# Kernel optimization log

Hardware: AMD Instinct MI355X
Metric: run time of the kernel (lower is better)

Reference implementation:

```python
import jax, jax.numpy as jnp
import numpy as np

D_MODEL = 1024
LAYER_IDX = 5
D_FF = 4096
SPARSITY = 0.9
TOKENS = 8192
IN_UP = D_MODEL * (LAYER_IDX + 1)  # 6144


def _sparse_weight(rng, out_f, in_f, sparsity):
    """Row-wise k-sparse weight matrix mimicking SparseLinear's padded-CSR:
    each output row keeps k = round(in_f*(1-sparsity)) live columns,
    values ~ U(-b, b) with b = 1/sqrt(effective_fan_in)."""
    k = max(1, round(in_f * (1.0 - sparsity)))
    bound = 1.0 / np.sqrt(max(1.0, in_f * (1.0 - sparsity)))
    scores = rng.random((out_f, in_f))
    # top-k per row -> boolean mask
    thresh = np.partition(scores, in_f - k, axis=1)[:, in_f - k][:, None]
    mask = scores >= thresh
    W = (rng.uniform(-bound, bound, (out_f, in_f)).astype(np.float32)) * mask
    return jnp.asarray(W), jnp.asarray(mask)


def setup_inputs() -> dict:
    key = jax.random.key(0)
    x = jax.random.normal(key, (TOKENS, IN_UP), dtype=jnp.float32)
    rng = np.random.default_rng(0)
    W_up, mask_up = _sparse_weight(rng, D_FF, IN_UP, SPARSITY)
    W_down, mask_down = _sparse_weight(rng, D_MODEL, D_FF, SPARSITY)
    return {"ffn_input_cat": x, "W_up": W_up, "W_down": W_down,
            "mask_up": mask_up, "mask_down": mask_down}


def reference(ffn_input_cat, W_up, W_down, mask_up, mask_down):
    # fc_down(gelu(fc_up(x))); SparseLinear == masked dense linear, no bias.
    # torch F.gelu default is the exact (erf) gelu.
    h = jax.nn.gelu(ffn_input_cat @ (W_up * mask_up).T, approximate=False)  # [T, d_ff]
    return h @ (W_down * mask_down).T  # [T, d_model]
```

## Files before the change

kernel.cpp:

```cpp
#include <hip/hip_runtime.h>
#include <cstdint>
#include <cstddef>

typedef unsigned short u16;
typedef __attribute__((ext_vector_type(8))) short  bf16x8;
typedef __attribute__((ext_vector_type(4))) float  f32x4;

__device__ __forceinline__ u16 f2bf(float f) {
    unsigned u = __float_as_uint(f);
    unsigned r = (u + 0x7FFFu + ((u >> 16) & 1u)) >> 16;
    return (u16)r;
}

__device__ __forceinline__ void async_lds16(const u16* g, u16* l) {
    __builtin_amdgcn_global_load_lds(
        (const __attribute__((address_space(1))) unsigned int*)g,
        (__attribute__((address_space(3))) unsigned int*)l,
        16, 0, 0);
}

__global__ __launch_bounds__(256) void cvt3_kernel(const float* __restrict__ s0, u16* __restrict__ d0, int n0,
                                                   const float* __restrict__ s1, u16* __restrict__ d1, int n1,
                                                   const float* __restrict__ s2, u16* __restrict__ d2, int n2) {
    int i = blockIdx.x * 256 + threadIdx.x;
    const float* s; u16* d;
    if (i < n0)            { s = s0; d = d0; }
    else if (i < n0 + n1)  { s = s1; d = d1; i -= n0; }
    else                   { s = s2; d = d2; i -= n0 + n1; if (i >= n2) return; }
    const float4* sp = (const float4*)s;
    float4 a = sp[2 * i];
    float4 b = sp[2 * i + 1];
    union { bf16x8 v; u16 e[8]; } o;
    o.e[0] = f2bf(a.x); o.e[1] = f2bf(a.y); o.e[2] = f2bf(a.z); o.e[3] = f2bf(a.w);
    o.e[4] = f2bf(b.x); o.e[5] = f2bf(b.y); o.e[6] = f2bf(b.z); o.e[7] = f2bf(b.w);
    ((bf16x8*)d)[i] = o.v;
}

#define BM 128
#define BN 128
#define BK 64

template<bool GELU, typename OutT>
__global__ __launch_bounds__(256) void gemm_bt(const u16* __restrict__ A,
                                               const u16* __restrict__ B,
                                               OutT* __restrict__ C,
                                               int M, int N, int K,
                                               int lda, int ldb, int ldc) {
    __shared__ __align__(16) u16 As[BM * BK];
    __shared__ __align__(16) u16 Bs[BN * BK];

    const int tid  = threadIdx.x;
    const int wave = tid >> 6;
    const int lane = tid & 63;
    const int quad = lane >> 4;
    const int r16  = lane & 15;

    const int n0 = blockIdx.x * BN;
    const int m0 = blockIdx.y * BM;

    const int wm = (wave >> 1) * 64;
    const int wn = (wave & 1) * 64;

    const int srow = tid >> 3;
    const int g8   = (tid & 7) ^ (srow & 7);
    const int scol = g8 * 8;

    const u16* gA[4]; const u16* gB[4];
    u16* lA[4]; u16* lB[4];
#pragma unroll
    for (int i = 0; i < 4; i++) {
        gA[i] = A + (size_t)(m0 + 32 * i + srow) * lda + scol;
        gB[i] = B + (size_t)(n0 + 32 * i + srow) * ldb + scol;
        lA[i] = &As[(32 * i + 8 * wave) * BK];
        lB[i] = &Bs[(32 * i + 8 * wave) * BK];
    }

    f32x4 acc[4][4] = {};

    for (int k0 = 0; k0 < K; k0 += BK) {
#pragma unroll
        for (int i = 0; i < 4; i++) async_lds16(gA[i] + k0, lA[i]);
#pragma unroll
        for (int i = 0; i < 4; i++) async_lds16(gB[i] + k0, lB[i]);
        __syncthreads();

#pragma unroll
        for (int ks = 0; ks < 2; ks++) {
            bf16x8 af[4], bf[4];
#pragma unroll
            for (int i = 0; i < 4; i++) {
                int ra = wm + i * 16 + r16;
                int rb = wn + i * 16 + r16;
                int pa = ((ks * 4 + quad) ^ (ra & 7)) * 8;
                int pb = ((ks * 4 + quad) ^ (rb & 7)) * 8;
                af[i] = *(const bf16x8*)&As[ra * BK + pa];
                bf[i] = *(const bf16x8*)&Bs[rb * BK + pb];
            }
#pragma unroll
            for (int mi = 0; mi < 4; mi++)
#pragma unroll
                for (int ni = 0; ni < 4; ni++)
                    acc[mi][ni] = __builtin_amdgcn_mfma_f32_16x16x32_bf16(
                        af[mi], bf[ni], acc[mi][ni], 0, 0, 0);
        }
        __syncthreads();
    }

#pragma unroll
    for (int mi = 0; mi < 4; mi++) {
#pragma unroll
        for (int r = 0; r < 4; r++) {
            size_t rowoff = (size_t)(m0 + wm + mi * 16 + quad * 4 + r) * ldc;
#pragma unroll
            for (int ni = 0; ni < 4; ni++) {
                int col = n0 + wn + ni * 16 + r16;
                float v = acc[mi][ni][r];
                if constexpr (GELU)
                    v = 0.5f * v * (1.0f + erff(v * 0.70710678118654752f));
                if constexpr (sizeof(OutT) == 2)
                    ((u16*)C)[rowoff + col] = f2bf(v);
                else
                    ((float*)C)[rowoff + col] = v;
            }
        }
    }
}

extern "C" void kernel_launch(void* const* d_in, const int* in_sizes, int n_in,
                              void* d_out, int out_size, void* d_ws, size_t ws_size,
                              hipStream_t stream) {
    const int T   = 8192;
    const int DIN = 6144;
    const int DFF = 4096;
    const int DM  = 1024;

    const float* x  = (const float*)d_in[0];
    const float* wu = (const float*)d_in[1];
    const float* wd = (const float*)d_in[2];

    u16* xb  = (u16*)d_ws;
    u16* wub = xb  + (size_t)T * DIN;
    u16* wdb = wub + (size_t)DFF * DIN;
    u16* hb  = wdb + (size_t)DM * DFF;

    const int n8x  = T * DIN / 8;
    const int n8wu = DFF * DIN / 8;
    const int n8wd = DM * DFF / 8;
    cvt3_kernel<<<(n8x + n8wu + n8wd) / 256, 256, 0, stream>>>(
        x, xb, n8x, wu, wub, n8wu, wd, wdb, n8wd);

    dim3 g1(DFF / BN, T / BM);
    gemm_bt<true, u16><<<g1, 256, 0, stream>>>(xb, wub, hb,
                                               T, DFF, DIN, DIN, DIN, DFF);

    dim3 g2(DM / BN, T / BM);
    gemm_bt<false, float><<<g2, 256, 0, stream>>>(hb, wdb, (float*)d_out,
                                                  T, DM, DFF, DFF, DFF, DM);
}
```

Measured before the change: 934.0 us.

## Rewrite GEMM as 256x256 tile, 8-wave, double-buffered async-LDS pipeline

Replaces the 128x128 single-buffered GEMM with a 256x256 tile kernel using 512 threads. K is split into 32-wide halves, double-buffered in LDS, and the next tiles are prefetched while MFMAs run. It also remaps workgroup order for L2 locality and raises MFMA priority with setprio. The aim is to hide global load latency and raise arithmetic intensity per byte loaded. The cost is more register pressure from 8x4 accumulators and a smaller grid for the second GEMM: only 128 workgroups.

```diff
diff --git a/kernel.cpp b/kernel.cpp
--- a/kernel.cpp
+++ b/kernel.cpp
@@ -36,18 +36,15 @@
     ((bf16x8*)d)[i] = o.v;
 }
 
-#define BM 128
-#define BN 128
-#define BK 64
+#define KHSZ (256 * 32)
 
 template<bool GELU, typename OutT>
-__global__ __launch_bounds__(256) void gemm_bt(const u16* __restrict__ A,
-                                               const u16* __restrict__ B,
-                                               OutT* __restrict__ C,
-                                               int M, int N, int K,
-                                               int lda, int ldb, int ldc) {
-    __shared__ __align__(16) u16 As[BM * BK];
-    __shared__ __align__(16) u16 Bs[BN * BK];
+__global__ __launch_bounds__(512, 2) void gemm256(const u16* __restrict__ A,
+                                                  const u16* __restrict__ B,
+                                                  OutT* __restrict__ C,
+                                                  int K, int lda, int ldb, int ldc) {
+    __shared__ __align__(16) u16 sA[2][2][KHSZ];
+    __shared__ __align__(16) u16 sB[2][2][KHSZ];
 
     const int tid  = threadIdx.x;
     const int wave = tid >> 6;
@@ -55,59 +52,106 @@
     const int quad = lane >> 4;
     const int r16  = lane & 15;
 
-    const int n0 = blockIdx.x * BN;
-    const int m0 = blockIdx.y * BM;
-
-    const int wm = (wave >> 1) * 64;
-    const int wn = (wave & 1) * 64;
-
-    const int srow = tid >> 3;
-    const int g8   = (tid & 7) ^ (srow & 7);
-    const int scol = g8 * 8;
-
-    const u16* gA[4]; const u16* gB[4];
-    u16* lA[4]; u16* lB[4];
+    const int nwg = gridDim.x * gridDim.y;
+    int lin = blockIdx.y * gridDim.x + blockIdx.x;
+    lin = (lin & 7) * (nwg >> 3) + (lin >> 3);
+    const int n0 = (lin % gridDim.x) * 256;
+    const int m0 = (lin / gridDim.x) * 256;
+
+    const int wm = (wave >> 2) * 128;
+    const int wn = (wave & 3) * 64;
+
+    const int srow = tid >> 2;
+    const int scol = ((tid & 3) ^ ((srow >> 1) & 3)) * 8;
+    const int ld0  = (wave * 16) * 32;
+    const int ld1  = (128 + wave * 16) * 32;
+
+    const u16* gA0 = A + (size_t)(m0 + srow) * lda + scol;
+    const u16* gA1 = A + (size_t)(m0 + 128 + srow) * lda + scol;
+    const u16* gB0 = B + (size_t)(n0 + srow) * ldb + scol;
+    const u16* gB1 = B + (size_t)(n0 + 128 + srow) * ldb + scol;
+
+#define STAGE_A(t, kh) { const int ko_ = (t) * 64 + (kh) * 32; u16* d_ = &sA[(t) & 1][kh][0]; \
+        async_lds16(gA0 + ko_, d_ + ld0); async_lds16(gA1 + ko_, d_ + ld1); }
+#define STAGE_B(t, kh) { const int ko_ = (t) * 64 + (kh) * 32; u16* d_ = &sB[(t) & 1][kh][0]; \
+        async_lds16(gB0 + ko_, d_ + ld0); async_lds16(gB1 + ko_, d_ + ld1); }
+
+    int oA[8], oB[4];
+#pragma unroll
+    for (int i = 0; i < 8; i++) {
+        int ra = wm + i * 16 + r16;
+        oA[i] = ra * 32 + ((quad ^ ((ra >> 1) & 3)) << 3);
+    }
 #pragma unroll
     for (int i = 0; i < 4; i++) {
-        gA[i] = A + (size_t)(m0 + 32 * i + srow) * lda + scol;
-        gB[i] = B + (size_t)(n0 + 32 * i + srow) * ldb + scol;
-        lA[i] = &As[(32 * i + 8 * wave) * BK];
-        lB[i] = &Bs[(32 * i + 8 * wave) * BK];
-    }
-
-    f32x4 acc[4][4] = {};
-
-    for (int k0 = 0; k0 < K; k0 += BK) {
-#pragma unroll
-        for (int i = 0; i < 4; i++) async_lds16(gA[i] + k0, lA[i]);
-#pragma unroll
-        for (int i = 0; i < 4; i++) async_lds16(gB[i] + k0, lB[i]);
-        __syncthreads();
-
-#pragma unroll
-        for (int ks = 0; ks < 2; ks++) {
-            bf16x8 af[4], bf[4];
-#pragma unroll
-            for (int i = 0; i < 4; i++) {
-                int ra = wm + i * 16 + r16;
-                int rb = wn + i * 16 + r16;
-                int pa = ((ks * 4 + quad) ^ (ra & 7)) * 8;
-                int pb = ((ks * 4 + quad) ^ (rb & 7)) * 8;
-                af[i] = *(const bf16x8*)&As[ra * BK + pa];
-                bf[i] = *(const bf16x8*)&Bs[rb * BK + pb];
-            }
-#pragma unroll
-            for (int mi = 0; mi < 4; mi++)
-#pragma unroll
-                for (int ni = 0; ni < 4; ni++)
-                    acc[mi][ni] = __builtin_amdgcn_mfma_f32_16x16x32_bf16(
-                        af[mi], bf[ni], acc[mi][ni], 0, 0, 0);
+        int rb = wn + i * 16 + r16;
+        oB[i] = rb * 32 + ((quad ^ ((rb >> 1) & 3)) << 3);
+    }
+
+    f32x4 acc[8][4] = {};
+    const int NT = K / 64;
+
+    STAGE_A(0, 0); STAGE_B(0, 0); STAGE_A(0, 1); STAGE_B(0, 1);
+    STAGE_A(1, 0); STAGE_B(1, 0);
+    asm volatile("s_waitcnt vmcnt(4)" ::: "memory");
+    __builtin_amdgcn_s_barrier();
+
+#define MFMA16(mbase, AF, BF) \
+    __builtin_amdgcn_s_barrier(); \
+    asm volatile("s_waitcnt lgkmcnt(0)" ::: "memory"); \
+    __builtin_amdgcn_sched_barrier(0); \
+    __builtin_amdgcn_s_setprio(1); \
+    _Pragma("unroll") \
+    for (int mi_ = 0; mi_ < 4; mi_++) \
+        _Pragma("unroll") \
+        for (int ni_ = 0; ni_ < 4; ni_++) \
+            acc[(mbase) + mi_][ni_] = __builtin_amdgcn_mfma_f32_16x16x32_bf16( \
+                AF[mi_], BF[ni_], acc[(mbase) + mi_][ni_], 0, 0, 0); \
+    __builtin_amdgcn_s_setprio(0); \
+    __builtin_amdgcn_sched_barrier(0);
+
+    for (int t = 0; t < NT; ++t) {
+        const u16* At0 = &sA[t & 1][0][0];
+        const u16* At1 = &sA[t & 1][1][0];
+        const u16* Bt0 = &sB[t & 1][0][0];
+        const u16* Bt1 = &sB[t & 1][1][0];
+        const int tn  = (t + 1 < NT) ? t + 1 : t + 1 - NT;
+        const int tn2 = (t + 2 < NT) ? t + 2 : t + 2 - NT;
+
+        bf16x8 af[4], bf[4];
+
+#pragma unroll
+        for (int i = 0; i < 4; i++) {
+            af[i] = *(const bf16x8*)&At0[oA[i]];
+            bf[i] = *(const bf16x8*)&Bt0[oB[i]];
         }
-        __syncthreads();
-    }
-
-#pragma unroll
-    for (int mi = 0; mi < 4; mi++) {
+        STAGE_A(tn, 1); STAGE_B(tn, 1);
+        MFMA16(0, af, bf);
+        __builtin_amdgcn_s_barrier();
+
+#pragma unroll
+        for (int i = 0; i < 4; i++) af[i] = *(const bf16x8*)&At0[oA[4 + i]];
+        MFMA16(4, af, bf);
+        __builtin_amdgcn_s_barrier();
+
+#pragma unroll
+        for (int i = 0; i < 4; i++) {
+            af[i] = *(const bf16x8*)&At1[oA[i]];
+            bf[i] = *(const bf16x8*)&Bt1[oB[i]];
+        }
+        STAGE_A(tn2, 0); STAGE_B(tn2, 0);
+        MFMA16(0, af, bf);
+        __builtin_amdgcn_s_barrier();
+
+#pragma unroll
+        for (int i = 0; i < 4; i++) af[i] = *(const bf16x8*)&At1[oA[4 + i]];
+        MFMA16(4, af, bf);
+        asm volatile("s_waitcnt vmcnt(4)" ::: "memory");
+        __builtin_amdgcn_s_barrier();
+    }
+
+#pragma unroll
+    for (int mi = 0; mi < 8; mi++) {
 #pragma unroll
         for (int r = 0; r < 4; r++) {
             size_t rowoff = (size_t)(m0 + wm + mi * 16 + quad * 4 + r) * ldc;
@@ -149,11 +193,10 @@
     cvt3_kernel<<<(n8x + n8wu + n8wd) / 256, 256, 0, stream>>>(
         x, xb, n8x, wu, wub, n8wu, wd, wdb, n8wd);
 
-    dim3 g1(DFF / BN, T / BM);
-    gemm_bt<true, u16><<<g1, 256, 0, stream>>>(xb, wub, hb,
-                                               T, DFF, DIN, DIN, DIN, DFF);
-
-    dim3 g2(DM / BN, T / BM);
-    gemm_bt<false, float><<<g2, 256, 0, stream>>>(hb, wdb, (float*)d_out,
-                                                  T, DM, DFF, DFF, DFF, DM);
-}
+    dim3 g1(DFF / 256, T / 256);
+    gemm256<true, u16><<<g1, 512, 0, stream>>>(xb, wub, hb, DIN, DIN, DIN, DFF);
+
+    dim3 g2(DM / 256, T / 256);
+    gemm256<false, float><<<g2, 512, 0, stream>>>(hb, wdb, (float*)d_out,
+                                                  DFF, DFF, DFF, DM);
+}
```

Measured after the change: 939.2 us. About the same (+0.6%).
